# Kernel tuning notes

Hardware: AMD Instinct MI355X
Metric: run time of the kernel (lower is better)

The kernel has to match this reference:

```python
import jax, jax.numpy as jnp
import numpy as np

B, S, E, H = 4, 2048, 1024, 16
DK = E // H  # 64


def setup_inputs() -> dict:
    key = jax.random.key(0)
    ks = jax.random.split(key, 6)
    scale = 1.0 / np.sqrt(E)
    return {
        "x": jax.random.normal(ks[0], (B, S, E), dtype=jnp.float32),
        "Wq": jax.random.normal(ks[1], (E, E), dtype=jnp.float32) * scale,
        "Wk": jax.random.normal(ks[2], (E, E), dtype=jnp.float32) * scale,
        "Wv": jax.random.normal(ks[3], (E, E), dtype=jnp.float32) * scale,
        "Wo": jax.random.normal(ks[4], (E, E), dtype=jnp.float32) * scale,
        "theta": jax.random.normal(ks[5], (DK,), dtype=jnp.float32),
    }


def _heads(t):
    # [B,S,E] -> [B,H,S,DK]
    b, s, _ = t.shape
    return t.reshape(b, s, H, DK).transpose(0, 2, 1, 3)


def reference(x, Wq, Wk, Wv, Wo, theta):
    # nn.Linear (no bias): y = x @ W.T
    # quantum transform: independent single-qubit RX(x)->RX(theta)->  <Z> = cos(x+theta)
    q = jnp.cos(_heads(x @ Wq.T) + theta)  # [B,H,S,DK]
    k = jnp.cos(_heads(x @ Wk.T) + theta)
    v = jnp.cos(_heads(x @ Wv.T) + theta)
    scores = jnp.einsum("bhqd,bhkd->bhqk", q, k) / jnp.sqrt(jnp.float32(DK))
    attn = jax.nn.softmax(scores, axis=-1)  # dropout is identity in eval
    out = jnp.einsum("bhqk,bhkd->bhqd", attn, v)  # [B,H,S,DK]
    out = out.transpose(0, 2, 1, 3).reshape(x.shape[0], -1, E)
    return out @ Wo.T
```

## Files before the change

kernel.cpp:

```cpp
#include <hip/hip_runtime.h>

#define B_  4
#define S_  2048
#define E_  1024
#define H_  16
#define DK_ 64
#define M_  (B_*S_)

typedef __attribute__((ext_vector_type(8)))  short short8;
typedef __attribute__((ext_vector_type(4)))  float f32x4;
typedef __attribute__((ext_vector_type(16))) float f32x16;

#define QSCALE 0.18033688f

__device__ __forceinline__ unsigned short f2b(float f) {
    union { float f; unsigned u; } v; v.f = f;
    unsigned u = v.u;
    return (unsigned short)((u + 0x7fffu + ((u >> 16) & 1u)) >> 16);
}

__device__ __forceinline__ void gload_lds16(const unsigned short* g, unsigned short* l) {
    __builtin_amdgcn_global_load_lds((const __attribute__((address_space(1))) void*)g,
                                     (__attribute__((address_space(3))) void*)l, 16, 0, 0);
}

#define XN4 (M_*E_/4)
#define WN4 (E_*E_/4)
__global__ __launch_bounds__(256) void cvt_all(
    const float* __restrict__ x,
    const float* __restrict__ w0, const float* __restrict__ w1,
    const float* __restrict__ w2, const float* __restrict__ w3,
    unsigned short* __restrict__ xb, unsigned short* __restrict__ wb,
    unsigned short* __restrict__ wob) {
    int i = blockIdx.x * 256 + threadIdx.x;
    const float* src;
    unsigned short* dst;
    int idx;
    if (i < XN4) { src = x; dst = xb; idx = i; }
    else {
        int j = i - XN4;
        int z = j >> 18;
        idx = j & (WN4 - 1);
        src = (z == 0) ? w0 : (z == 1) ? w1 : (z == 2) ? w2 : w3;
        dst = (z < 3) ? wb + (size_t)z * E_ * E_ : wob;
    }
    float4 f = ((const float4*)src)[idx];
    ushort4 o;
    o.x = f2b(f.x); o.y = f2b(f.y); o.z = f2b(f.z); o.w = f2b(f.w);
    ((ushort4*)dst)[idx] = o;
}

__global__ __launch_bounds__(256) void gemm_qkv(
    const unsigned short* __restrict__ xb,
    const unsigned short* __restrict__ Wb,
    const float* __restrict__ theta,
    unsigned short* __restrict__ qb,
    unsigned short* __restrict__ kb,
    unsigned short* __restrict__ vtb)
{
    __shared__ unsigned short smem[128*144];
    unsigned short* As = smem;
    unsigned short* Bs = smem + 128*64;
    const int tid = threadIdx.x;
    const int w = tid >> 6, lane = tid & 63, quad = lane >> 4, col = lane & 15;
    const int wm = (w & 1) * 64, wn = (w >> 1) * 64;
    const int m0 = blockIdx.x * 128, n0 = blockIdx.y * 128, z = blockIdx.z;
    const unsigned short* Wz = Wb + (size_t)z * E_ * E_;
    const int srow = lane >> 3;
    const int sch  = ((lane & 7) ^ srow) * 8;
    const int rsw  = col & 7;

    f32x4 acc[4][4] = {};
    for (int k0 = 0; k0 < E_; k0 += 64) {
        #pragma unroll
        for (int c = 0; c < 4; c++) {
            int row = w*32 + c*8 + srow;
            gload_lds16(&xb[(size_t)(m0+row)*E_ + k0 + sch], &As[(w*32 + c*8)*64]);
            gload_lds16(&Wz[(size_t)(n0+row)*E_ + k0 + sch], &Bs[(w*32 + c*8)*64]);
        }
        __syncthreads();
        #pragma unroll
        for (int kk = 0; kk < 64; kk += 32) {
            short8 a[4], b[4];
            #pragma unroll
            for (int i = 0; i < 4; i++)
                a[i] = *(const short8*)&As[(wm + i*16 + col)*64 + ((((kk>>3) + quad) ^ rsw) * 8)];
            #pragma unroll
            for (int j = 0; j < 4; j++)
                b[j] = *(const short8*)&Bs[(wn + j*16 + col)*64 + ((((kk>>3) + quad) ^ rsw) * 8)];
            #pragma unroll
            for (int i = 0; i < 4; i++)
                #pragma unroll
                for (int j = 0; j < 4; j++)
                    acc[i][j] = __builtin_amdgcn_mfma_f32_16x16x32_bf16(a[i], b[j], acc[i][j], 0, 0, 0);
        }
        __syncthreads();
    }

    const int bblk = m0 >> 11;
    const int sbase = m0 & (S_-1);

    if (z != 2) {
        const float qs = (z == 0) ? QSCALE : 1.0f;
        #pragma unroll
        for (int j = 0; j < 4; j++) {
            int nl = wn + j*16 + col;
            float th = theta[(n0 + nl) & 63];
            #pragma unroll
            for (int i = 0; i < 4; i++)
                #pragma unroll
                for (int r = 0; r < 4; r++) {
                    int ml = wm + i*16 + quad*4 + r;
                    int nls = nl ^ (((ml >> 2) & 3) << 4);
                    smem[ml*144 + nls] = f2b(__cosf(acc[i][j][r] + th) * qs);
                }
        }
        __syncthreads();
        unsigned short* dst = (z == 0) ? qb : kb;
        const int h0 = n0 >> 6;
        #pragma unroll
        for (int k = 0; k < 8; k++) {
            int idx = k*256 + tid;
            int chunk = idx & 7, seg = idx >> 3;
            int ml = seg >> 1, hh = seg & 1;
            int ch = chunk ^ (((ml >> 2) & 3) << 1);
            int4 val = *(const int4*)&smem[ml*144 + hh*64 + ch*8];
            size_t g = ((size_t)(bblk*H_ + h0 + hh)*S_ + sbase + ml)*DK_ + chunk*8;
            *(int4*)&dst[g] = val;
        }
    } else {
        #pragma unroll
        for (int j = 0; j < 4; j++) {
            int nl = wn + j*16 + col;
            float th = theta[(n0 + nl) & 63];
            #pragma unroll
            for (int i = 0; i < 4; i++)
                #pragma unroll
                for (int r = 0; r < 4; r++)
                    smem[nl*136 + wm + i*16 + quad*4 + r] = f2b(__cosf(acc[i][j][r] + th));
        }
        __syncthreads();
        int row = tid >> 1, halfm = (tid & 1) * 64;
        int n = n0 + row, h = n >> 6, d = n & 63;
        size_t base = ((size_t)(bblk*H_ + h)*DK_ + d)*S_ + sbase + halfm;
        #pragma unroll
        for (int k = 0; k < 8; k++)
            *(int4*)&vtb[base + k*8] = *(const int4*)&smem[row*136 + halfm + k*8];
    }
}

__global__ __launch_bounds__(256) void gemm_out(
    const unsigned short* __restrict__ ctx,
    const unsigned short* __restrict__ Wob,
    float* __restrict__ out)
{
    __shared__ unsigned short As[128*64];
    __shared__ unsigned short Bs[128*64];
    const int tid = threadIdx.x;
    const int w = tid >> 6, lane = tid & 63, quad = lane >> 4, col = lane & 15;
    const int wm = (w & 1) * 64, wn = (w >> 1) * 64;
    const int m0 = blockIdx.x * 128, n0 = blockIdx.y * 128;
    const int srow = lane >> 3;
    const int sch  = ((lane & 7) ^ srow) * 8;
    const int rsw  = col & 7;

    f32x4 acc[4][4] = {};
    for (int k0 = 0; k0 < E_; k0 += 64) {
        #pragma unroll
        for (int c = 0; c < 4; c++) {
            int row = w*32 + c*8 + srow;
            gload_lds16(&ctx[(size_t)(m0+row)*E_ + k0 + sch], &As[(w*32 + c*8)*64]);
            gload_lds16(&Wob[(size_t)(n0+row)*E_ + k0 + sch], &Bs[(w*32 + c*8)*64]);
        }
        __syncthreads();
        #pragma unroll
        for (int kk = 0; kk < 64; kk += 32) {
            short8 a[4], b[4];
            #pragma unroll
            for (int i = 0; i < 4; i++)
                a[i] = *(const short8*)&As[(wm + i*16 + col)*64 + ((((kk>>3) + quad) ^ rsw) * 8)];
            #pragma unroll
            for (int j = 0; j < 4; j++)
                b[j] = *(const short8*)&Bs[(wn + j*16 + col)*64 + ((((kk>>3) + quad) ^ rsw) * 8)];
            #pragma unroll
            for (int i = 0; i < 4; i++)
                #pragma unroll
                for (int j = 0; j < 4; j++)
                    acc[i][j] = __builtin_amdgcn_mfma_f32_16x16x32_bf16(a[i], b[j], acc[i][j], 0, 0, 0);
        }
        __syncthreads();
    }
    #pragma unroll
    for (int j = 0; j < 4; j++) {
        int n = n0 + wn + j*16 + col;
        #pragma unroll
        for (int i = 0; i < 4; i++)
            #pragma unroll
            for (int r = 0; r < 4; r++) {
                int m = m0 + wm + i*16 + quad*4 + r;
                out[(size_t)m*E_ + n] = acc[i][j][r];
            }
    }
}

#define LPK 72
#define LPV 136
#define KVB 128

__global__ __launch_bounds__(256, 2) void flash_attn(
    const unsigned short* __restrict__ qb,
    const unsigned short* __restrict__ kb,
    const unsigned short* __restrict__ vtb,
    unsigned short* __restrict__ ctx)
{
    __shared__ unsigned short Kt[2][KVB*LPK];
    __shared__ unsigned short Vt[2][64*LPV];
    const int tid = threadIdx.x;
    const int w = tid >> 6, lane = tid & 63, col = lane & 31, half = lane >> 5;

    const int f   = blockIdx.y * gridDim.x + blockIdx.x;
    const int swz = (f & 7) * 64 + (f >> 3);
    const int q0  = (swz & 7) * 256;
    const int bh  = swz >> 3;

    const unsigned short* kbase = kb  + (size_t)bh * S_ * DK_;
    const unsigned short* vbase = vtb + (size_t)bh * DK_ * S_;

    short8 qf[2][4];
    {
        const unsigned short* qrow = qb + ((size_t)bh*S_ + q0 + w*64 + col)*DK_;
        #pragma unroll
        for (int s = 0; s < 2; s++)
            #pragma unroll
            for (int c = 0; c < 4; c++)
                qf[s][c] = *(const short8*)&qrow[(size_t)s*32*DK_ + c*16 + half*8];
    }

    union U8 { unsigned u[4]; short8 s8; };
    U8 ones;
    #pragma unroll
    for (int i = 0; i < 4; i++) ones.u[i] = 0x3F803F80u;

    f32x16 oacc[2][2] = {};
    f32x16 lacc[2] = {};

    #pragma unroll
    for (int j = 0; j < 4; j++) {
        int s = tid + j*256;
        int krow = s >> 3, kc8 = (s & 7) * 8;
        int vrow = s >> 4, vc8 = (s & 15) * 8;
        *(int4*)&Kt[0][krow*LPK + kc8] = *(const int4*)&kbase[(size_t)krow*DK_ + kc8];
        *(int4*)&Vt[0][vrow*LPV + vc8] = *(const int4*)&vbase[(size_t)vrow*S_ + vc8];
    }
    __syncthreads();

    for (int it = 0; it < S_/KVB; ++it) {
        const int cur = it & 1, nxt = cur ^ 1;
        const int ktn = it*KVB + KVB;
        int4 rk[4], rv[4];
        if (ktn < S_) {
            #pragma unroll
            for (int j = 0; j < 4; j++) {
                int s = tid + j*256;
                int krow = s >> 3, kc8 = (s & 7) * 8;
                int vrow = s >> 4, vc8 = (s & 15) * 8;
                rk[j] = *(const int4*)&kbase[(size_t)(ktn + krow)*DK_ + kc8];
                rv[j] = *(const int4*)&vbase[(size_t)vrow*S_ + ktn + vc8];
            }
        }

        #pragma unroll
        for (int t = 0; t < 4; t++) {
            f32x16 sa0 = {}, sa1 = {};
            __builtin_amdgcn_s_setprio(1);
            #pragma unroll
            for (int c = 0; c < 4; c++) {
                short8 kf = *(const short8*)&Kt[cur][(t*32 + col)*LPK + c*16 + half*8];
                sa0 = __builtin_amdgcn_mfma_f32_32x32x16_bf16(kf, qf[0][c], sa0, 0, 0, 0);
                sa1 = __builtin_amdgcn_mfma_f32_32x32x16_bf16(kf, qf[1][c], sa1, 0, 0, 0);
            }
            __builtin_amdgcn_s_setprio(0);
            unsigned pk[2][4][2];
            #pragma unroll
            for (int rg = 0; rg < 4; rg++) {
                float a0 = __builtin_amdgcn_exp2f(sa0[rg*4+0]);
                float a1 = __builtin_amdgcn_exp2f(sa0[rg*4+1]);
                float a2 = __builtin_amdgcn_exp2f(sa0[rg*4+2]);
                float a3 = __builtin_amdgcn_exp2f(sa0[rg*4+3]);
                pk[0][rg][0] = __builtin_amdgcn_perm(__float_as_uint(a1), __float_as_uint(a0), 0x07060302u);
                pk[0][rg][1] = __builtin_amdgcn_perm(__float_as_uint(a3), __float_as_uint(a2), 0x07060302u);
                float b0 = __builtin_amdgcn_exp2f(sa1[rg*4+0]);
                float b1 = __builtin_amdgcn_exp2f(sa1[rg*4+1]);
                float b2 = __builtin_amdgcn_exp2f(sa1[rg*4+2]);
                float b3 = __builtin_amdgcn_exp2f(sa1[rg*4+3]);
                pk[1][rg][0] = __builtin_amdgcn_perm(__float_as_uint(b1), __float_as_uint(b0), 0x07060302u);
                pk[1][rg][1] = __builtin_amdgcn_perm(__float_as_uint(b3), __float_as_uint(b2), 0x07060302u);
            }
            #pragma unroll
            for (int kc = 0; kc < 2; kc++) {
                const int lo = 2*kc, hi = 2*kc + 1;
                U8 pa[2];
                #pragma unroll
                for (int s = 0; s < 2; s++) {
                    auto s0 = __builtin_amdgcn_permlane32_swap((int)pk[s][lo][0], (int)pk[s][hi][0], false, false);
                    auto s1 = __builtin_amdgcn_permlane32_swap((int)pk[s][lo][1], (int)pk[s][hi][1], false, false);
                    pa[s].u[0] = (unsigned)s0[0];
                    pa[s].u[1] = (unsigned)s1[0];
                    pa[s].u[2] = (unsigned)s0[1];
                    pa[s].u[3] = (unsigned)s1[1];
                }
                __builtin_amdgcn_s_setprio(1);
                lacc[0] = __builtin_amdgcn_mfma_f32_32x32x16_bf16(pa[0].s8, ones.s8, lacc[0], 0, 0, 0);
                lacc[1] = __builtin_amdgcn_mfma_f32_32x32x16_bf16(pa[1].s8, ones.s8, lacc[1], 0, 0, 0);
                #pragma unroll
                for (int dt = 0; dt < 2; dt++) {
                    short8 vf = *(const short8*)&Vt[cur][(dt*32 + col)*LPV + t*32 + kc*16 + half*8];
                    oacc[0][dt] = __builtin_amdgcn_mfma_f32_32x32x16_bf16(pa[0].s8, vf, oacc[0][dt], 0, 0, 0);
                    oacc[1][dt] = __builtin_amdgcn_mfma_f32_32x32x16_bf16(pa[1].s8, vf, oacc[1][dt], 0, 0, 0);
                }
                __builtin_amdgcn_s_setprio(0);
            }
        }

        if (ktn < S_) {
            #pragma unroll
            for (int j = 0; j < 4; j++) {
                int s = tid + j*256;
                int krow = s >> 3, kc8 = (s & 7) * 8;
                int vrow = s >> 4, vc8 = (s & 15) * 8;
                *(int4*)&Kt[nxt][krow*LPK + kc8] = rk[j];
                *(int4*)&Vt[nxt][vrow*LPV + vc8] = rv[j];
            }
        }
        __syncthreads();
    }

    const int b = bh >> 4, h = bh & 15;
    #pragma unroll
    for (int s = 0; s < 2; s++)
        #pragma unroll
        for (int rg = 0; rg < 4; rg++)
            #pragma unroll
            for (int rr = 0; rr < 4; rr++) {
                int row = rr + rg*8 + half*4;
                float inv = 1.0f / lacc[s][rg*4 + rr];
                int sq = q0 + w*64 + s*32 + row;
                size_t rowoff = ((size_t)(b*S_ + sq))*E_ + h*64;
                #pragma unroll
                for (int dt = 0; dt < 2; dt++)
                    ctx[rowoff + dt*32 + col] = f2b(oacc[s][dt][rg*4 + rr] * inv);
            }
}

extern "C" void kernel_launch(void* const* d_in, const int* in_sizes, int n_in,
                              void* d_out, int out_size, void* d_ws, size_t ws_size,
                              hipStream_t stream) {
    (void)in_sizes; (void)n_in; (void)out_size; (void)ws_size;
    const float* x     = (const float*)d_in[0];
    const float* Wq    = (const float*)d_in[1];
    const float* Wk    = (const float*)d_in[2];
    const float* Wv    = (const float*)d_in[3];
    const float* Wo    = (const float*)d_in[4];
    const float* theta = (const float*)d_in[5];
    float* out = (float*)d_out;

    unsigned short* ws  = (unsigned short*)d_ws;
    unsigned short* xb  = ws;
    unsigned short* Wb  = xb  + (size_t)M_*E_;
    unsigned short* Wob = Wb  + (size_t)3*E_*E_;
    unsigned short* qb  = Wob + (size_t)E_*E_;
    unsigned short* kb  = qb  + (size_t)B_*H_*S_*DK_;
    unsigned short* vtb = kb  + (size_t)B_*H_*S_*DK_;
    unsigned short* ctx = xb;

    cvt_all<<<(XN4 + 4*WN4)/256, 256, 0, stream>>>(x, Wq, Wk, Wv, Wo, xb, Wb, Wob);

    gemm_qkv<<<dim3(M_/128, E_/128, 3), 256, 0, stream>>>(xb, Wb, theta, qb, kb, vtb);
    flash_attn<<<dim3(S_/256, B_*H_), 256, 0, stream>>>(qb, kb, vtb, ctx);
    gemm_out<<<dim3(M_/128, E_/128), 256, 0, stream>>>(ctx, Wob, out);
}
```

Before: 257.0 us.

## Double-buffer LDS tiles in QKV and output GEMMs to overlap loads with MFMA

Both projection GEMMs now use two LDS buffers: the next K-slice is loaded asynchronously into one buffer while MFMAs consume the other, which hides global-load latency behind compute. A union reuses the same LDS for the epilogue staging. MFMA sections are also wrapped in s_setprio to raise wave priority during math. The cost is doubled LDS per block (64 KB), which may reduce occupancy.

```diff
diff --git a/kernel.cpp b/kernel.cpp
--- a/kernel.cpp
+++ b/kernel.cpp
@@ -50,6 +50,44 @@
     ((ushort4*)dst)[idx] = o;
 }
 
+union GemmShm {
+    struct { unsigned short As0[8192], Bs0[8192], As1[8192], Bs1[8192]; } kl;
+    unsigned short epi[18432];
+};
+
+__device__ __forceinline__ void gemm_stage(
+    const unsigned short* Ag, const unsigned short* Bg,
+    unsigned short* As, unsigned short* Bs, int w, int srow, int sch) {
+    #pragma unroll
+    for (int c = 0; c < 4; c++) {
+        int ro = (w*32 + c*8 + srow);
+        gload_lds16(Ag + (size_t)ro*E_ + sch, As + (w*32 + c*8)*64);
+        gload_lds16(Bg + (size_t)ro*E_ + sch, Bs + (w*32 + c*8)*64);
+    }
+}
+
+__device__ __forceinline__ void gemm_compute(
+    const unsigned short* As, const unsigned short* Bs,
+    f32x4 (&acc)[4][4], int wm, int wn, int col, int quad, int rsw) {
+    #pragma unroll
+    for (int kk = 0; kk < 64; kk += 32) {
+        short8 a[4], b[4];
+        #pragma unroll
+        for (int i = 0; i < 4; i++)
+            a[i] = *(const short8*)&As[(wm + i*16 + col)*64 + ((((kk>>3) + quad) ^ rsw) * 8)];
+        #pragma unroll
+        for (int j = 0; j < 4; j++)
+            b[j] = *(const short8*)&Bs[(wn + j*16 + col)*64 + ((((kk>>3) + quad) ^ rsw) * 8)];
+        __builtin_amdgcn_s_setprio(1);
+        #pragma unroll
+        for (int i = 0; i < 4; i++)
+            #pragma unroll
+            for (int j = 0; j < 4; j++)
+                acc[i][j] = __builtin_amdgcn_mfma_f32_16x16x32_bf16(a[i], b[j], acc[i][j], 0, 0, 0);
+        __builtin_amdgcn_s_setprio(0);
+    }
+}
+
 __global__ __launch_bounds__(256) void gemm_qkv(
     const unsigned short* __restrict__ xb,
     const unsigned short* __restrict__ Wb,
@@ -58,9 +96,7 @@
     unsigned short* __restrict__ kb,
     unsigned short* __restrict__ vtb)
 {
-    __shared__ unsigned short smem[128*144];
-    unsigned short* As = smem;
-    unsigned short* Bs = smem + 128*64;
+    __shared__ GemmShm shm;
     const int tid = threadIdx.x;
     const int w = tid >> 6, lane = tid & 63, quad = lane >> 4, col = lane & 15;
     const int wm = (w & 1) * 64, wn = (w >> 1) * 64;
@@ -70,33 +106,23 @@
     const int sch  = ((lane & 7) ^ srow) * 8;
     const int rsw  = col & 7;
 
+    const unsigned short* Ag = xb + (size_t)m0 * E_;
+    const unsigned short* Bg = Wz + (size_t)n0 * E_;
+
     f32x4 acc[4][4] = {};
-    for (int k0 = 0; k0 < E_; k0 += 64) {
-        #pragma unroll
-        for (int c = 0; c < 4; c++) {
-            int row = w*32 + c*8 + srow;
-            gload_lds16(&xb[(size_t)(m0+row)*E_ + k0 + sch], &As[(w*32 + c*8)*64]);
-            gload_lds16(&Wz[(size_t)(n0+row)*E_ + k0 + sch], &Bs[(w*32 + c*8)*64]);
-        }
-        __syncthreads();
-        #pragma unroll
-        for (int kk = 0; kk < 64; kk += 32) {
-            short8 a[4], b[4];
-            #pragma unroll
-            for (int i = 0; i < 4; i++)
-                a[i] = *(const short8*)&As[(wm + i*16 + col)*64 + ((((kk>>3) + quad) ^ rsw) * 8)];
-            #pragma unroll
-            for (int j = 0; j < 4; j++)
-                b[j] = *(const short8*)&Bs[(wn + j*16 + col)*64 + ((((kk>>3) + quad) ^ rsw) * 8)];
-            #pragma unroll
-            for (int i = 0; i < 4; i++)
-                #pragma unroll
-                for (int j = 0; j < 4; j++)
-                    acc[i][j] = __builtin_amdgcn_mfma_f32_16x16x32_bf16(a[i], b[j], acc[i][j], 0, 0, 0);
-        }
-        __syncthreads();
-    }
-
+    gemm_stage(Ag, Bg, shm.kl.As0, shm.kl.Bs0, w, srow, sch);
+    __syncthreads();
+    for (int k0 = 0; k0 < E_; k0 += 128) {
+        gemm_stage(Ag + k0 + 64, Bg + k0 + 64, shm.kl.As1, shm.kl.Bs1, w, srow, sch);
+        gemm_compute(shm.kl.As0, shm.kl.Bs0, acc, wm, wn, col, quad, rsw);
+        __syncthreads();
+        if (k0 + 128 < E_)
+            gemm_stage(Ag + k0 + 128, Bg + k0 + 128, shm.kl.As0, shm.kl.Bs0, w, srow, sch);
+        gemm_compute(shm.kl.As1, shm.kl.Bs1, acc, wm, wn, col, quad, rsw);
+        __syncthreads();
+    }
+
+    unsigned short* ep = shm.epi;
     const int bblk = m0 >> 11;
     const int sbase = m0 & (S_-1);
 
@@ -112,7 +138,7 @@
                 for (int r = 0; r < 4; r++) {
                     int ml = wm + i*16 + quad*4 + r;
                     int nls = nl ^ (((ml >> 2) & 3) << 4);
-                    smem[ml*144 + nls] = f2b(__cosf(acc[i][j][r] + th) * qs);
+                    ep[ml*144 + nls] = f2b(__cosf(acc[i][j][r] + th) * qs);
                 }
         }
         __syncthreads();
@@ -124,7 +150,7 @@
             int chunk = idx & 7, seg = idx >> 3;
             int ml = seg >> 1, hh = seg & 1;
             int ch = chunk ^ (((ml >> 2) & 3) << 1);
-            int4 val = *(const int4*)&smem[ml*144 + hh*64 + ch*8];
+            int4 val = *(const int4*)&ep[ml*144 + hh*64 + ch*8];
             size_t g = ((size_t)(bblk*H_ + h0 + hh)*S_ + sbase + ml)*DK_ + chunk*8;
             *(int4*)&dst[g] = val;
         }
@@ -137,7 +163,7 @@
             for (int i = 0; i < 4; i++)
                 #pragma unroll
                 for (int r = 0; r < 4; r++)
-                    smem[nl*136 + wm + i*16 + quad*4 + r] = f2b(__cosf(acc[i][j][r] + th));
+                    ep[nl*136 + wm + i*16 + quad*4 + r] = f2b(__cosf(acc[i][j][r] + th));
         }
         __syncthreads();
         int row = tid >> 1, halfm = (tid & 1) * 64;
@@ -145,7 +171,7 @@
         size_t base = ((size_t)(bblk*H_ + h)*DK_ + d)*S_ + sbase + halfm;
         #pragma unroll
         for (int k = 0; k < 8; k++)
-            *(int4*)&vtb[base + k*8] = *(const int4*)&smem[row*136 + halfm + k*8];
+            *(int4*)&vtb[base + k*8] = *(const int4*)&ep[row*136 + halfm + k*8];
     }
 }
 
@@ -154,8 +180,7 @@
     const unsigned short* __restrict__ Wob,
     float* __restrict__ out)
 {
-    __shared__ unsigned short As[128*64];
-    __shared__ unsigned short Bs[128*64];
+    __shared__ GemmShm shm;
     const int tid = threadIdx.x;
     const int w = tid >> 6, lane = tid & 63, quad = lane >> 4, col = lane & 15;
     const int wm = (w & 1) * 64, wn = (w >> 1) * 64;
@@ -164,30 +189,19 @@
     const int sch  = ((lane & 7) ^ srow) * 8;
     const int rsw  = col & 7;
 
+    const unsigned short* Ag = ctx + (size_t)m0 * E_;
+    const unsigned short* Bg = Wob + (size_t)n0 * E_;
+
     f32x4 acc[4][4] = {};
-    for (int k0 = 0; k0 < E_; k0 += 64) {
-        #pragma unroll
-        for (int c = 0; c < 4; c++) {
-            int row = w*32 + c*8 + srow;
-            gload_lds16(&ctx[(size_t)(m0+row)*E_ + k0 + sch], &As[(w*32 + c*8)*64]);
-            gload_lds16(&Wob[(size_t)(n0+row)*E_ + k0 + sch], &Bs[(w*32 + c*8)*64]);
-        }
-        __syncthreads();
-        #pragma unroll
-        for (int kk = 0; kk < 64; kk += 32) {
-            short8 a[4], b[4];
-            #pragma unroll
-            for (int i = 0; i < 4; i++)
-                a[i] = *(const short8*)&As[(wm + i*16 + col)*64 + ((((kk>>3) + quad) ^ rsw) * 8)];
-            #pragma unroll
-            for (int j = 0; j < 4; j++)
-                b[j] = *(const short8*)&Bs[(wn + j*16 + col)*64 + ((((kk>>3) + quad) ^ rsw) * 8)];
-            #pragma unroll
-            for (int i = 0; i < 4; i++)
-                #pragma unroll
-                for (int j = 0; j < 4; j++)
-                    acc[i][j] = __builtin_amdgcn_mfma_f32_16x16x32_bf16(a[i], b[j], acc[i][j], 0, 0, 0);
-        }
+    gemm_stage(Ag, Bg, shm.kl.As0, shm.kl.Bs0, w, srow, sch);
+    __syncthreads();
+    for (int k0 = 0; k0 < E_; k0 += 128) {
+        gemm_stage(Ag + k0 + 64, Bg + k0 + 64, shm.kl.As1, shm.kl.Bs1, w, srow, sch);
+        gemm_compute(shm.kl.As0, shm.kl.Bs0, acc, wm, wn, col, quad, rsw);
+        __syncthreads();
+        if (k0 + 128 < E_)
+            gemm_stage(Ag + k0 + 128, Bg + k0 + 128, shm.kl.As0, shm.kl.Bs0, w, srow, sch);
+        gemm_compute(shm.kl.As1, shm.kl.Bs1, acc, wm, wn, col, quad, rsw);
         __syncthreads();
     }
     #pragma unroll
```

After: 247.2 us. 1.04x faster.
